# Optimization experiments

Hardware: AMD Instinct MI355X
Metric: run time of the kernel (lower is better)

## Reference

```python
import jax, jax.numpy as jnp
import numpy as np

H = 64  # hidden_size
IN = 1  # input_size
OUT = 7  # output_size
B, T = 4096, 512


def setup_inputs() -> dict:
    key = jax.random.key(0)
    ks = jax.random.split(key, 11)
    s = 1.0 / np.sqrt(H)  # PyTorch LSTM init scale
    u = lambda k, shp: jax.random.uniform(k, shp, jnp.float32, -s, s)
    return {
        "x": jax.random.normal(ks[0], (B, T, IN), jnp.float32),
        # layer 0
        "Wih0": u(ks[1], (4 * H, IN)),
        "Whh0": u(ks[2], (4 * H, H)),
        "bih0": u(ks[3], (4 * H,)),
        "bhh0": u(ks[4], (4 * H,)),
        # layer 1
        "Wih1": u(ks[5], (4 * H, H)),
        "Whh1": u(ks[6], (4 * H, H)),
        "bih1": u(ks[7], (4 * H,)),
        "bhh1": u(ks[8], (4 * H,)),
        # fc head
        "Wfc": u(ks[9], (OUT, H)),
        "bfc": u(ks[10], (OUT,)),
    }


def _lstm_layer(x, Wih, Whh, bih, bhh):
    """x: [B, T, F] -> hidden sequence [B, T, H]. PyTorch gate order i,f,g,o."""
    b, t, _ = x.shape
    h = Whh.shape[1]
    # precompute input contribution for all timesteps: [T, B, 4H]
    xg = (jnp.einsum('btf,gf->btg', x, Wih) + bih + bhh).transpose(1, 0, 2)
    WhhT = Whh.T  # [H, 4H]

    def step(carry, g_t):
        h_t, c_t = carry
        gates = g_t + h_t @ WhhT  # [B, 4H]
        i, f, g, o = jnp.split(gates, 4, axis=-1)
        i = jax.nn.sigmoid(i)
        f = jax.nn.sigmoid(f)
        g = jnp.tanh(g)
        o = jax.nn.sigmoid(o)
        c_new = f * c_t + i * g
        h_new = o * jnp.tanh(c_new)
        return (h_new, c_new), h_new

    h0 = jnp.zeros((b, h), x.dtype)
    c0 = jnp.zeros((b, h), x.dtype)
    (_, _), hs = jax.lax.scan(step, (h0, c0), xg)
    return hs.transpose(1, 0, 2)  # [B, T, H]


def reference(x, Wih0, Whh0, bih0, bhh0, Wih1, Whh1, bih1, bhh1, Wfc, bfc):
    h1 = _lstm_layer(x, Wih0, Whh0, bih0, bhh0)   # dropout between layers is identity in eval
    h2 = _lstm_layer(h1, Wih1, Whh1, bih1, bhh1)
    last = h2[:, -1, :]  # [B, H]; dropout identity in eval
    return last @ Wfc.T + bfc  # [B, OUT]
```

## Files before the change

### kernel.cpp

```cpp
#include <hip/hip_runtime.h>
#include <hip/hip_bf16.h>

#define HH 64
#define TT 512
#define BB 8

typedef __attribute__((ext_vector_type(8))) short short8;
typedef __attribute__((ext_vector_type(4))) float f32x4;

static __device__ __forceinline__ unsigned short f2bf(float f) {
  unsigned u = __float_as_uint(f);
  u += 0x7fffu + ((u >> 16) & 1u);
  return (unsigned short)(u >> 16);
}

static __device__ __forceinline__ float sigm(float x) {
  float e = __builtin_amdgcn_exp2f(-1.442695041f * x);
  return __builtin_amdgcn_rcpf(1.0f + e);
}
static __device__ __forceinline__ float tanh_fast(float x) {
  float e = __builtin_amdgcn_exp2f(2.885390082f * x);
  return 1.0f - 2.0f * __builtin_amdgcn_rcpf(1.0f + e);
}

static __device__ __forceinline__ short8 pack8(const float* __restrict__ p) {
  const float4* p4 = (const float4*)p;
  float4 a = p4[0], b = p4[1];
  short8 r;
  r[0] = (short)f2bf(a.x); r[1] = (short)f2bf(a.y);
  r[2] = (short)f2bf(a.z); r[3] = (short)f2bf(a.w);
  r[4] = (short)f2bf(b.x); r[5] = (short)f2bf(b.y);
  r[6] = (short)f2bf(b.z); r[7] = (short)f2bf(b.w);
  return r;
}

#define MF(A, B, C) __builtin_amdgcn_mfma_f32_16x16x32_bf16((A), (B), (C), 0, 0, 0)

#define ACT_STORE(A0, A1, A2, A3, J, XV, HASX, CSTv, WROv, WRB, LASTF) {       \
    float pi = (A0)[J], pf = (A1)[J], pg = (A2)[J], po = (A3)[J];              \
    if (HASX) {                                                                \
      pi = fmaf((XV), wx[0], pi); pf = fmaf((XV), wx[1], pf);                  \
      pg = fmaf((XV), wx[2], pg); po = fmaf((XV), wx[3], po);                  \
    }                                                                          \
    float iv = sigm(pi), fv = sigm(pf);                                        \
    float gv = tanh_fast(pg), ov = sigm(po);                                   \
    float c = fmaf(fv, (CSTv), iv * gv);                                       \
    (CSTv) = c;                                                                \
    float h = ov * tanh_fast(c);                                               \
    *(__hip_bfloat16*)((WRB) + (WROv)) = __float2bfloat16(h);                  \
    if (LASTF) h1f[(2 * q + (J) / 2) * HH + colw] = h;                         \
  }

#define STEP_A(P) {                                                            \
    const char* rd = (const char*)h0buf[(P) ^ 1];                              \
    short8 af0 = *(const short8*)(rd + rdo0);                                  \
    short8 af1 = *(const short8*)(rd + rdo1);                                  \
    float2 xv = *(const float2*)xpf; xpf += BB;                                \
    f32x4 a0 = MF(af0, wf[0], bs[0]); a0 = MF(af1, wf[1], a0);                 \
    f32x4 a1 = MF(af0, wf[2], bs[1]); a1 = MF(af1, wf[3], a1);                 \
    f32x4 a2 = MF(af0, wf[4], bs[2]); a2 = MF(af1, wf[5], a2);                 \
    f32x4 a3 = MF(af0, wf[6], bs[3]); a3 = MF(af1, wf[7], a3);                 \
    char* wrb = (char*)h0buf[P];                                               \
    ACT_STORE(a0, a1, a2, a3, 0, xv.x, true, cst0, wro0, wrb, false)           \
    ACT_STORE(a0, a1, a2, a3, 2, xv.y, true, cst1, wro1, wrb, false)           \
  }

#define STEP_B(P, LAST) {                                                      \
    const char* rd0 = (const char*)h0buf[(P) ^ 1];                             \
    const char* rd1 = (const char*)h1buf[P];                                   \
    short8 af0 = *(const short8*)(rd0 + rdo0);                                 \
    short8 af1 = *(const short8*)(rd0 + rdo1);                                 \
    short8 af2 = *(const short8*)(rd1 + rdo0);                                 \
    short8 af3 = *(const short8*)(rd1 + rdo1);                                 \
    f32x4 a0 = MF(af0, wf[0],  bs[0]); a0 = MF(af1, wf[1],  a0);               \
    a0 = MF(af2, wf[2],  a0);  a0 = MF(af3, wf[3],  a0);                       \
    f32x4 a1 = MF(af0, wf[4],  bs[1]); a1 = MF(af1, wf[5],  a1);               \
    a1 = MF(af2, wf[6],  a1);  a1 = MF(af3, wf[7],  a1);                       \
    f32x4 a2 = MF(af0, wf[8],  bs[2]); a2 = MF(af1, wf[9],  a2);               \
    a2 = MF(af2, wf[10], a2);  a2 = MF(af3, wf[11], a2);                       \
    f32x4 a3 = MF(af0, wf[12], bs[3]); a3 = MF(af1, wf[13], a3);               \
    a3 = MF(af2, wf[14], a3);  a3 = MF(af3, wf[15], a3);                       \
    char* wrb = (char*)h1buf[(P) ^ 1];                                         \
    ACT_STORE(a0, a1, a2, a3, 0, 0.f, false, cst0, wro0, wrb, LAST)            \
    ACT_STORE(a0, a1, a2, a3, 2, 0.f, false, cst1, wro1, wrb, LAST)            \
  }

__global__ __launch_bounds__(512, 4)
void lstm2_fused(const float* __restrict__ x,
                 const float* __restrict__ Wih0, const float* __restrict__ Whh0,
                 const float* __restrict__ bih0, const float* __restrict__ bhh0,
                 const float* __restrict__ Wih1, const float* __restrict__ Whh1,
                 const float* __restrict__ bih1, const float* __restrict__ bhh1,
                 const float* __restrict__ Wfc,  const float* __restrict__ bfc,
                 float* __restrict__ out)
{
  __shared__ float xs[TT * BB];
  __shared__ __align__(16) unsigned short h0buf[2][16 * HH];
  __shared__ __align__(16) unsigned short h1buf[2][16 * HH];
  __shared__ float h1f[BB * HH];

  const int tid  = threadIdx.x;
  const int wave = tid >> 6;
  const int lane = tid & 63;
  const int grp  = wave >> 2;
  const int w    = wave & 3;
  const int m    = lane & 15;
  const int q    = lane >> 4;
  const int b0   = blockIdx.x * BB;

  {
    const int t = tid;
    #pragma unroll
    for (int r = 0; r < BB; ++r)
      xs[t * BB + r] = x[(size_t)(b0 + r) * TT + t];
  }
  ((unsigned int*)h0buf)[tid] = 0; ((unsigned int*)h0buf)[tid + 512] = 0;
  ((unsigned int*)h1buf)[tid] = 0; ((unsigned int*)h1buf)[tid + 512] = 0;

  short8 wf[16];
  f32x4 bs[4];
  float wx[4];
  #pragma unroll
  for (int n = 0; n < 4; ++n) {
    const int colg = 16 * (4 * n + w) + m;
    if (grp == 0) {
      const float b = bih0[colg] + bhh0[colg];
      bs[n][0] = b; bs[n][1] = b; bs[n][2] = b; bs[n][3] = b;
      wx[n] = Wih0[colg];
      #pragma unroll
      for (int kt = 0; kt < 2; ++kt)
        wf[n * 2 + kt] = pack8(Whh0 + colg * HH + kt * 32 + q * 8);
    } else {
      const float b = bih1[colg] + bhh1[colg];
      bs[n][0] = b; bs[n][1] = b; bs[n][2] = b; bs[n][3] = b;
      wx[n] = 0.f;
      #pragma unroll
      for (int kt = 0; kt < 4; ++kt) {
        const float* Wsrc = (kt < 2) ? Wih1 : Whh1;
        wf[n * 4 + kt] = pack8(Wsrc + colg * HH + (kt & 1) * 32 + q * 8);
      }
    }
  }

  const int colw = 16 * w + m;
  const int rdo0 = m * 128 + ((q * 16) ^ ((m & 7) << 4));
  const int rdo1 = m * 128 + ((64 + q * 16) ^ ((m & 7) << 4));
  const int r0 = 4 * q;
  const int r2 = 4 * q + 2;
  const int wro0 = r0 * 128 + ((2 * colw) ^ ((r0 & 7) << 4));
  const int wro1 = r2 * 128 + ((2 * colw) ^ ((r2 & 7) << 4));

  __syncthreads();

  float cst0 = 0.f, cst1 = 0.f;
  const float* xpf = xs + 2 * q;

  if (grp == 0) { STEP_A(0) }
  __syncthreads();

  #pragma unroll 1
  for (int k = 0; k < (TT - 2) / 2; ++k) {
    if (grp == 0) { STEP_A(1) } else { STEP_B(1, false) }
    __syncthreads();
    if (grp == 0) { STEP_A(0) } else { STEP_B(0, false) }
    __syncthreads();
  }
  if (grp == 0) { STEP_A(1) } else { STEP_B(1, false) }
  __syncthreads();
  if (grp == 1) { STEP_B(0, true) }
  __syncthreads();

  if (tid < BB * 7) {
    const int b = tid / 7, o = tid % 7;
    float s = bfc[o];
    #pragma unroll
    for (int k = 0; k < HH; ++k) s = fmaf(h1f[b * HH + k], Wfc[o * HH + k], s);
    out[(size_t)(b0 + b) * 7 + o] = s;
  }
}

extern "C" void kernel_launch(void* const* d_in, const int* in_sizes, int n_in,
                              void* d_out, int out_size, void* d_ws, size_t ws_size,
                              hipStream_t stream) {
  const float* x    = (const float*)d_in[0];
  const float* Wih0 = (const float*)d_in[1];
  const float* Whh0 = (const float*)d_in[2];
  const float* bih0 = (const float*)d_in[3];
  const float* bhh0 = (const float*)d_in[4];
  const float* Wih1 = (const float*)d_in[5];
  const float* Whh1 = (const float*)d_in[6];
  const float* bih1 = (const float*)d_in[7];
  const float* bhh1 = (const float*)d_in[8];
  const float* Wfc  = (const float*)d_in[9];
  const float* bfc  = (const float*)d_in[10];
  float* out = (float*)d_out;

  dim3 grid(4096 / BB);
  dim3 block(512);
  hipLaunchKernelGGL(lstm2_fused, grid, block, 0, stream,
                     x, Wih0, Whh0, bih0, bhh0, Wih1, Whh1, bih1, bhh1, Wfc, bfc, out);
}
```

Before: 426.3 us.

## Merge both LSTM layers into each wave and fold activation scaling into weights

Each of 4 waves now computes both layer 0 and layer 1 for its columns, replacing the two 4-wave groups, so the block shrinks from 512 to 256 threads. The log2(e) and 2*log2(e) factors are folded into the bf16 weights and biases. The gate activations are rewritten with exp2 and combined rationals that use fewer reciprocals, processed as 2-wide vectors. The goal is to cut transcendental and reciprocal count and barrier participants, at the cost of more registers per wave, a longer serial path per wave, and possible precision changes from the clamped exponentials.

```diff
diff --git a/kernel.cpp b/kernel.cpp
--- a/kernel.cpp
+++ b/kernel.cpp
@@ -7,6 +7,10 @@
 
 typedef __attribute__((ext_vector_type(8))) short short8;
 typedef __attribute__((ext_vector_type(4))) float f32x4;
+typedef __attribute__((ext_vector_type(2))) float f32x2;
+
+#define K1 1.4426950408889634f
+#define K2 2.8853900817779268f
 
 static __device__ __forceinline__ unsigned short f2bf(float f) {
   unsigned u = __float_as_uint(f);
@@ -14,78 +18,90 @@
   return (unsigned short)(u >> 16);
 }
 
-static __device__ __forceinline__ float sigm(float x) {
-  float e = __builtin_amdgcn_exp2f(-1.442695041f * x);
-  return __builtin_amdgcn_rcpf(1.0f + e);
-}
-static __device__ __forceinline__ float tanh_fast(float x) {
-  float e = __builtin_amdgcn_exp2f(2.885390082f * x);
-  return 1.0f - 2.0f * __builtin_amdgcn_rcpf(1.0f + e);
-}
-
-static __device__ __forceinline__ short8 pack8(const float* __restrict__ p) {
-  const float4* p4 = (const float4*)p;
-  float4 a = p4[0], b = p4[1];
+static __device__ __forceinline__ short8 pack8s(const float* __restrict__ p, float s) {
   short8 r;
-  r[0] = (short)f2bf(a.x); r[1] = (short)f2bf(a.y);
-  r[2] = (short)f2bf(a.z); r[3] = (short)f2bf(a.w);
-  r[4] = (short)f2bf(b.x); r[5] = (short)f2bf(b.y);
-  r[6] = (short)f2bf(b.z); r[7] = (short)f2bf(b.w);
+  #pragma unroll
+  for (int i = 0; i < 8; ++i) r[i] = (short)f2bf(p[i] * s);
   return r;
 }
 
+static __device__ __forceinline__ f32x2 splat2(float b) { f32x2 r; r[0] = b; r[1] = b; return r; }
+static __device__ __forceinline__ f32x2 vexp2(f32x2 v) {
+  f32x2 r; r[0] = __builtin_amdgcn_exp2f(v[0]); r[1] = __builtin_amdgcn_exp2f(v[1]); return r;
+}
+static __device__ __forceinline__ f32x2 vrcp(f32x2 v) {
+  f32x2 r; r[0] = __builtin_amdgcn_rcpf(v[0]); r[1] = __builtin_amdgcn_rcpf(v[1]); return r;
+}
+static __device__ __forceinline__ f32x2 vmin(f32x2 a, float b) {
+  return __builtin_elementwise_min(a, splat2(b));
+}
+
+static __device__ __forceinline__ f32x2 lstm_act2(f32x2 zi, f32x2 zf, f32x2 zg,
+                                                  f32x2 zo, f32x2& c) {
+  f32x2 Ei = vexp2(vmin(zi, 16.f));
+  f32x2 Ef = vexp2(vmin(zf, 16.f));
+  f32x2 G  = vexp2(vmin(zg, 23.f));
+  f32x2 Eo = vexp2(vmin(zo, 16.f));
+  f32x2 Pi = Ei + 1.f, Pf = Ef + 1.f, Pg = G + 1.f, Gm = G - 1.f;
+  f32x2 t2 = Pi * Pg;
+  f32x2 N  = Ef * c * t2 + Ei * Gm * Pf;
+  f32x2 D  = Pf * t2;
+  c = N * vrcp(D);
+  f32x2 C2 = vexp2(vmin(c * K2, 23.f));
+  f32x2 num = Eo * (C2 - 1.f);
+  f32x2 den = (Eo + 1.f) * (C2 + 1.f);
+  return num * vrcp(den);
+}
+
 #define MF(A, B, C) __builtin_amdgcn_mfma_f32_16x16x32_bf16((A), (B), (C), 0, 0, 0)
 
-#define ACT_STORE(A0, A1, A2, A3, J, XV, HASX, CSTv, WROv, WRB, LASTF) {       \
-    float pi = (A0)[J], pf = (A1)[J], pg = (A2)[J], po = (A3)[J];              \
-    if (HASX) {                                                                \
-      pi = fmaf((XV), wx[0], pi); pf = fmaf((XV), wx[1], pf);                  \
-      pg = fmaf((XV), wx[2], pg); po = fmaf((XV), wx[3], po);                  \
+#define STEP(P, DO_A, DO_B, LASTF) {                                           \
+    const char* h0r = (const char*)h0buf[(P) ^ 1];                             \
+    const char* h1r = (const char*)h1buf[P];                                   \
+    short8 af0 = *(const short8*)(h0r + rdo0);                                 \
+    short8 af1 = *(const short8*)(h0r + rdo1);                                 \
+    short8 af2 = *(const short8*)(h1r + rdo0);                                 \
+    short8 af3 = *(const short8*)(h1r + rdo1);                                 \
+    if (DO_A) {                                                                \
+      f32x4 a0 = MF(af0, wfA[0], bsA[0]); a0 = MF(af1, wfA[1], a0);            \
+      f32x4 a1 = MF(af0, wfA[2], bsA[1]); a1 = MF(af1, wfA[3], a1);            \
+      f32x4 a2 = MF(af0, wfA[4], bsA[2]); a2 = MF(af1, wfA[5], a2);            \
+      f32x4 a3 = MF(af0, wfA[6], bsA[3]); a3 = MF(af1, wfA[7], a3);            \
+      f32x2 xv = *(const f32x2*)xpf; xpf += BB;                                \
+      f32x2 zi = {a0[0], a0[2]}; zi += xv * wxs[0];                            \
+      f32x2 zf = {a1[0], a1[2]}; zf += xv * wxs[1];                            \
+      f32x2 zg = {a2[0], a2[2]}; zg += xv * wxs[2];                            \
+      f32x2 zo = {a3[0], a3[2]}; zo += xv * wxs[3];                            \
+      f32x2 hA = lstm_act2(zi, zf, zg, zo, cA);                                \
+      char* h0w = (char*)h0buf[P];                                             \
+      *(__hip_bfloat16*)(h0w + wro0) = __float2bfloat16(hA[0]);                \
+      *(__hip_bfloat16*)(h0w + wro1) = __float2bfloat16(hA[1]);                \
     }                                                                          \
-    float iv = sigm(pi), fv = sigm(pf);                                        \
-    float gv = tanh_fast(pg), ov = sigm(po);                                   \
-    float c = fmaf(fv, (CSTv), iv * gv);                                       \
-    (CSTv) = c;                                                                \
-    float h = ov * tanh_fast(c);                                               \
-    *(__hip_bfloat16*)((WRB) + (WROv)) = __float2bfloat16(h);                  \
-    if (LASTF) h1f[(2 * q + (J) / 2) * HH + colw] = h;                         \
-  }
-
-#define STEP_A(P) {                                                            \
-    const char* rd = (const char*)h0buf[(P) ^ 1];                              \
-    short8 af0 = *(const short8*)(rd + rdo0);                                  \
-    short8 af1 = *(const short8*)(rd + rdo1);                                  \
-    float2 xv = *(const float2*)xpf; xpf += BB;                                \
-    f32x4 a0 = MF(af0, wf[0], bs[0]); a0 = MF(af1, wf[1], a0);                 \
-    f32x4 a1 = MF(af0, wf[2], bs[1]); a1 = MF(af1, wf[3], a1);                 \
-    f32x4 a2 = MF(af0, wf[4], bs[2]); a2 = MF(af1, wf[5], a2);                 \
-    f32x4 a3 = MF(af0, wf[6], bs[3]); a3 = MF(af1, wf[7], a3);                 \
-    char* wrb = (char*)h0buf[P];                                               \
-    ACT_STORE(a0, a1, a2, a3, 0, xv.x, true, cst0, wro0, wrb, false)           \
-    ACT_STORE(a0, a1, a2, a3, 2, xv.y, true, cst1, wro1, wrb, false)           \
-  }
-
-#define STEP_B(P, LAST) {                                                      \
-    const char* rd0 = (const char*)h0buf[(P) ^ 1];                             \
-    const char* rd1 = (const char*)h1buf[P];                                   \
-    short8 af0 = *(const short8*)(rd0 + rdo0);                                 \
-    short8 af1 = *(const short8*)(rd0 + rdo1);                                 \
-    short8 af2 = *(const short8*)(rd1 + rdo0);                                 \
-    short8 af3 = *(const short8*)(rd1 + rdo1);                                 \
-    f32x4 a0 = MF(af0, wf[0],  bs[0]); a0 = MF(af1, wf[1],  a0);               \
-    a0 = MF(af2, wf[2],  a0);  a0 = MF(af3, wf[3],  a0);                       \
-    f32x4 a1 = MF(af0, wf[4],  bs[1]); a1 = MF(af1, wf[5],  a1);               \
-    a1 = MF(af2, wf[6],  a1);  a1 = MF(af3, wf[7],  a1);                       \
-    f32x4 a2 = MF(af0, wf[8],  bs[2]); a2 = MF(af1, wf[9],  a2);               \
-    a2 = MF(af2, wf[10], a2);  a2 = MF(af3, wf[11], a2);                       \
-    f32x4 a3 = MF(af0, wf[12], bs[3]); a3 = MF(af1, wf[13], a3);               \
-    a3 = MF(af2, wf[14], a3);  a3 = MF(af3, wf[15], a3);                       \
-    char* wrb = (char*)h1buf[(P) ^ 1];                                         \
-    ACT_STORE(a0, a1, a2, a3, 0, 0.f, false, cst0, wro0, wrb, LAST)            \
-    ACT_STORE(a0, a1, a2, a3, 2, 0.f, false, cst1, wro1, wrb, LAST)            \
-  }
-
-__global__ __launch_bounds__(512, 4)
+    if (DO_B) {                                                                \
+      f32x4 b0 = MF(af0, wfB[0],  bsB[0]); b0 = MF(af1, wfB[1],  b0);          \
+      b0 = MF(af2, wfB[2],  b0);  b0 = MF(af3, wfB[3],  b0);                   \
+      f32x4 b1 = MF(af0, wfB[4],  bsB[1]); b1 = MF(af1, wfB[5],  b1);          \
+      b1 = MF(af2, wfB[6],  b1);  b1 = MF(af3, wfB[7],  b1);                   \
+      f32x4 b2 = MF(af0, wfB[8],  bsB[2]); b2 = MF(af1, wfB[9],  b2);          \
+      b2 = MF(af2, wfB[10], b2);  b2 = MF(af3, wfB[11], b2);                   \
+      f32x4 b3 = MF(af0, wfB[12], bsB[3]); b3 = MF(af1, wfB[13], b3);          \
+      b3 = MF(af2, wfB[14], b3);  b3 = MF(af3, wfB[15], b3);                   \
+      f32x2 wi = {b0[0], b0[2]};                                               \
+      f32x2 wff = {b1[0], b1[2]};                                              \
+      f32x2 wg = {b2[0], b2[2]};                                               \
+      f32x2 wo = {b3[0], b3[2]};                                               \
+      f32x2 hB = lstm_act2(wi, wff, wg, wo, cB);                               \
+      char* h1w = (char*)h1buf[(P) ^ 1];                                       \
+      *(__hip_bfloat16*)(h1w + wro0) = __float2bfloat16(hB[0]);                \
+      *(__hip_bfloat16*)(h1w + wro1) = __float2bfloat16(hB[1]);                \
+      if (LASTF) {                                                             \
+        h1f[(2 * q) * HH + colw]     = hB[0];                                  \
+        h1f[(2 * q + 1) * HH + colw] = hB[1];                                  \
+      }                                                                        \
+    }                                                                          \
+  }
+
+__global__ __launch_bounds__(256, 2)
 void lstm2_fused(const float* __restrict__ x,
                  const float* __restrict__ Wih0, const float* __restrict__ Whh0,
                  const float* __restrict__ bih0, const float* __restrict__ bhh0,
@@ -102,42 +118,43 @@
   const int tid  = threadIdx.x;
   const int wave = tid >> 6;
   const int lane = tid & 63;
-  const int grp  = wave >> 2;
-  const int w    = wave & 3;
+  const int w    = wave;
   const int m    = lane & 15;
   const int q    = lane >> 4;
   const int b0   = blockIdx.x * BB;
 
-  {
-    const int t = tid;
+  for (int t = tid; t < TT; t += 256) {
     #pragma unroll
     for (int r = 0; r < BB; ++r)
       xs[t * BB + r] = x[(size_t)(b0 + r) * TT + t];
   }
-  ((unsigned int*)h0buf)[tid] = 0; ((unsigned int*)h0buf)[tid + 512] = 0;
-  ((unsigned int*)h1buf)[tid] = 0; ((unsigned int*)h1buf)[tid + 512] = 0;
-
-  short8 wf[16];
-  f32x4 bs[4];
-  float wx[4];
+  #pragma unroll
+  for (int i = 0; i < 4; ++i) ((unsigned int*)h0buf)[tid + 256 * i] = 0;
+  #pragma unroll
+  for (int i = 0; i < 4; ++i) ((unsigned int*)h1buf)[tid + 256 * i] = 0;
+
+  short8 wfA[8], wfB[16];
+  f32x4 bsA[4], bsB[4];
+  f32x2 wxs[4];
   #pragma unroll
   for (int n = 0; n < 4; ++n) {
+    const float s = (n == 2) ? K2 : K1;
     const int colg = 16 * (4 * n + w) + m;
-    if (grp == 0) {
-      const float b = bih0[colg] + bhh0[colg];
-      bs[n][0] = b; bs[n][1] = b; bs[n][2] = b; bs[n][3] = b;
-      wx[n] = Wih0[colg];
+    {
+      const float b = (bih0[colg] + bhh0[colg]) * s;
+      bsA[n][0] = b; bsA[n][1] = b; bsA[n][2] = b; bsA[n][3] = b;
+      wxs[n] = splat2(Wih0[colg] * s);
       #pragma unroll
       for (int kt = 0; kt < 2; ++kt)
-        wf[n * 2 + kt] = pack8(Whh0 + colg * HH + kt * 32 + q * 8);
-    } else {
-      const float b = bih1[colg] + bhh1[colg];
-      bs[n][0] = b; bs[n][1] = b; bs[n][2] = b; bs[n][3] = b;
-      wx[n] = 0.f;
+        wfA[n * 2 + kt] = pack8s(Whh0 + colg * HH + kt * 32 + q * 8, s);
+    }
+    {
+      const float b = (bih1[colg] + bhh1[colg]) * s;
+      bsB[n][0] = b; bsB[n][1] = b; bsB[n][2] = b; bsB[n][3] = b;
       #pragma unroll
       for (int kt = 0; kt < 4; ++kt) {
         const float* Wsrc = (kt < 2) ? Wih1 : Whh1;
-        wf[n * 4 + kt] = pack8(Wsrc + colg * HH + (kt & 1) * 32 + q * 8);
+        wfB[n * 4 + kt] = pack8s(Wsrc + colg * HH + (kt & 1) * 32 + q * 8, s);
       }
     }
   }
@@ -152,22 +169,22 @@
 
   __syncthreads();
 
-  float cst0 = 0.f, cst1 = 0.f;
+  f32x2 cA = splat2(0.f), cB = splat2(0.f);
   const float* xpf = xs + 2 * q;
 
-  if (grp == 0) { STEP_A(0) }
+  STEP(0, true, false, false)
   __syncthreads();
 
   #pragma unroll 1
   for (int k = 0; k < (TT - 2) / 2; ++k) {
-    if (grp == 0) { STEP_A(1) } else { STEP_B(1, false) }
+    STEP(1, true, true, false)
     __syncthreads();
-    if (grp == 0) { STEP_A(0) } else { STEP_B(0, false) }
+    STEP(0, true, true, false)
     __syncthreads();
   }
-  if (grp == 0) { STEP_A(1) } else { STEP_B(1, false) }
-  __syncthreads();
-  if (grp == 1) { STEP_B(0, true) }
+  STEP(1, true, true, false)
+  __syncthreads();
+  STEP(0, false, true, true)
   __syncthreads();
 
   if (tid < BB * 7) {
@@ -196,7 +213,7 @@
   float* out = (float*)d_out;
 
   dim3 grid(4096 / BB);
-  dim3 block(512);
+  dim3 block(256);
   hipLaunchKernelGGL(lstm2_fused, grid, block, 0, stream,
                      x, Wih0, Whh0, bih0, bhh0, Wih1, Whh1, bih1, bhh1, Wfc, bfc, out);
 }
```

After: 466.0 us. 1.09x slower.

## Fill all 16 MFMA rows with batch and fuse LSTM activations algebraically

Applied to the files above, without the earlier changes.

Doubles the batch tile per block from 8 to 16, so all 16 M-rows of the 16x16x32 MFMA carry real batch rows instead of half being wasted. The grid halves and each lane now updates four cell states. The gate activations are rewritten as a single rational expression built from exp2 results, which cuts the number of reciprocals per cell. The log2(e) scale factors are folded into the weights and biases at load time, and the math runs on packed float2 vectors. The trade-offs are fewer blocks per CU to hide the serial recurrence latency, and clamps on the exponent inputs to avoid overflow.

```diff
diff --git a/kernel.cpp b/kernel.cpp
--- a/kernel.cpp
+++ b/kernel.cpp
@@ -3,10 +3,14 @@
 
 #define HH 64
 #define TT 512
-#define BB 8
+#define BB 16
 
 typedef __attribute__((ext_vector_type(8))) short short8;
 typedef __attribute__((ext_vector_type(4))) float f32x4;
+typedef __attribute__((ext_vector_type(2))) float f32x2;
+
+#define K1 1.4426950408889634f
+#define K2 2.8853900817779268f
 
 static __device__ __forceinline__ unsigned short f2bf(float f) {
   unsigned u = __float_as_uint(f);
@@ -14,55 +18,73 @@
   return (unsigned short)(u >> 16);
 }
 
-static __device__ __forceinline__ float sigm(float x) {
-  float e = __builtin_amdgcn_exp2f(-1.442695041f * x);
-  return __builtin_amdgcn_rcpf(1.0f + e);
-}
-static __device__ __forceinline__ float tanh_fast(float x) {
-  float e = __builtin_amdgcn_exp2f(2.885390082f * x);
-  return 1.0f - 2.0f * __builtin_amdgcn_rcpf(1.0f + e);
-}
-
-static __device__ __forceinline__ short8 pack8(const float* __restrict__ p) {
-  const float4* p4 = (const float4*)p;
-  float4 a = p4[0], b = p4[1];
+static __device__ __forceinline__ short8 pack8s(const float* __restrict__ p, float s) {
   short8 r;
-  r[0] = (short)f2bf(a.x); r[1] = (short)f2bf(a.y);
-  r[2] = (short)f2bf(a.z); r[3] = (short)f2bf(a.w);
-  r[4] = (short)f2bf(b.x); r[5] = (short)f2bf(b.y);
-  r[6] = (short)f2bf(b.z); r[7] = (short)f2bf(b.w);
+  #pragma unroll
+  for (int i = 0; i < 8; ++i) r[i] = (short)f2bf(p[i] * s);
   return r;
 }
 
+static __device__ __forceinline__ f32x2 splat2(float b) { f32x2 r; r[0] = b; r[1] = b; return r; }
+static __device__ __forceinline__ f32x2 vexp2(f32x2 v) {
+  f32x2 r; r[0] = __builtin_amdgcn_exp2f(v[0]); r[1] = __builtin_amdgcn_exp2f(v[1]); return r;
+}
+static __device__ __forceinline__ f32x2 vrcp(f32x2 v) {
+  f32x2 r; r[0] = __builtin_amdgcn_rcpf(v[0]); r[1] = __builtin_amdgcn_rcpf(v[1]); return r;
+}
+static __device__ __forceinline__ f32x2 vmin2(f32x2 a, float b) {
+  return __builtin_elementwise_min(a, splat2(b));
+}
+
+static __device__ __forceinline__ f32x2 lstm_act2(f32x2 zi, f32x2 zf, f32x2 zg,
+                                                  f32x2 zo, f32x2& c) {
+  f32x2 Ei = vexp2(vmin2(zi, 16.f));
+  f32x2 Ef = vexp2(vmin2(zf, 16.f));
+  f32x2 G  = vexp2(vmin2(zg, 23.f));
+  f32x2 Eo = vexp2(vmin2(zo, 16.f));
+  f32x2 Pi = Ei + 1.f, Pf = Ef + 1.f, Pg = G + 1.f, Gm = G - 1.f;
+  f32x2 t2 = Pi * Pg;
+  f32x2 N  = Ef * c * t2 + Ei * Gm * Pf;
+  f32x2 D  = Pf * t2;
+  c = N * vrcp(D);
+  f32x2 C2 = vexp2(vmin2(c * K2, 23.f));
+  f32x2 num = Eo * (C2 - 1.f);
+  f32x2 den = (Eo + 1.f) * (C2 + 1.f);
+  return num * vrcp(den);
+}
+
 #define MF(A, B, C) __builtin_amdgcn_mfma_f32_16x16x32_bf16((A), (B), (C), 0, 0, 0)
-
-#define ACT_STORE(A0, A1, A2, A3, J, XV, HASX, CSTv, WROv, WRB, LASTF) {       \
-    float pi = (A0)[J], pf = (A1)[J], pg = (A2)[J], po = (A3)[J];              \
-    if (HASX) {                                                                \
-      pi = fmaf((XV), wx[0], pi); pf = fmaf((XV), wx[1], pf);                  \
-      pg = fmaf((XV), wx[2], pg); po = fmaf((XV), wx[3], po);                  \
-    }                                                                          \
-    float iv = sigm(pi), fv = sigm(pf);                                        \
-    float gv = tanh_fast(pg), ov = sigm(po);                                   \
-    float c = fmaf(fv, (CSTv), iv * gv);                                       \
-    (CSTv) = c;                                                                \
-    float h = ov * tanh_fast(c);                                               \
-    *(__hip_bfloat16*)((WRB) + (WROv)) = __float2bfloat16(h);                  \
-    if (LASTF) h1f[(2 * q + (J) / 2) * HH + colw] = h;                         \
-  }
 
 #define STEP_A(P) {                                                            \
     const char* rd = (const char*)h0buf[(P) ^ 1];                              \
     short8 af0 = *(const short8*)(rd + rdo0);                                  \
     short8 af1 = *(const short8*)(rd + rdo1);                                  \
-    float2 xv = *(const float2*)xpf; xpf += BB;                                \
+    f32x4 xv = *(const f32x4*)xpf; xpf += BB;                                  \
     f32x4 a0 = MF(af0, wf[0], bs[0]); a0 = MF(af1, wf[1], a0);                 \
     f32x4 a1 = MF(af0, wf[2], bs[1]); a1 = MF(af1, wf[3], a1);                 \
     f32x4 a2 = MF(af0, wf[4], bs[2]); a2 = MF(af1, wf[5], a2);                 \
     f32x4 a3 = MF(af0, wf[6], bs[3]); a3 = MF(af1, wf[7], a3);                 \
     char* wrb = (char*)h0buf[P];                                               \
-    ACT_STORE(a0, a1, a2, a3, 0, xv.x, true, cst0, wro0, wrb, false)           \
-    ACT_STORE(a0, a1, a2, a3, 2, xv.y, true, cst1, wro1, wrb, false)           \
+    {                                                                          \
+      f32x2 xp2 = {xv[0], xv[1]};                                              \
+      f32x2 zi = {a0[0], a0[1]}; zi += xp2 * wxs[0];                           \
+      f32x2 zf = {a1[0], a1[1]}; zf += xp2 * wxs[1];                           \
+      f32x2 zg = {a2[0], a2[1]}; zg += xp2 * wxs[2];                           \
+      f32x2 zo = {a3[0], a3[1]}; zo += xp2 * wxs[3];                           \
+      f32x2 h2 = lstm_act2(zi, zf, zg, zo, cst01);                             \
+      *(__hip_bfloat16*)(wrb + wro[0]) = __float2bfloat16(h2[0]);              \
+      *(__hip_bfloat16*)(wrb + wro[1]) = __float2bfloat16(h2[1]);              \
+    }                                                                          \
+    {                                                                          \
+      f32x2 xp2 = {xv[2], xv[3]};                                              \
+      f32x2 zi = {a0[2], a0[3]}; zi += xp2 * wxs[0];                           \
+      f32x2 zf = {a1[2], a1[3]}; zf += xp2 * wxs[1];                           \
+      f32x2 zg = {a2[2], a2[3]}; zg += xp2 * wxs[2];                           \
+      f32x2 zo = {a3[2], a3[3]}; zo += xp2 * wxs[3];                           \
+      f32x2 h2 = lstm_act2(zi, zf, zg, zo, cst23);                             \
+      *(__hip_bfloat16*)(wrb + wro[2]) = __float2bfloat16(h2[0]);              \
+      *(__hip_bfloat16*)(wrb + wro[3]) = __float2bfloat16(h2[1]);              \
+    }                                                                          \
   }
 
 #define STEP_B(P, LAST) {                                                      \
@@ -81,11 +103,31 @@
     f32x4 a3 = MF(af0, wf[12], bs[3]); a3 = MF(af1, wf[13], a3);               \
     a3 = MF(af2, wf[14], a3);  a3 = MF(af3, wf[15], a3);                       \
     char* wrb = (char*)h1buf[(P) ^ 1];                                         \
-    ACT_STORE(a0, a1, a2, a3, 0, 0.f, false, cst0, wro0, wrb, LAST)            \
-    ACT_STORE(a0, a1, a2, a3, 2, 0.f, false, cst1, wro1, wrb, LAST)            \
-  }
-
-__global__ __launch_bounds__(512, 4)
+    {                                                                          \
+      f32x2 zi = {a0[0], a0[1]}, zf = {a1[0], a1[1]};                          \
+      f32x2 zg = {a2[0], a2[1]}, zo = {a3[0], a3[1]};                          \
+      f32x2 h2 = lstm_act2(zi, zf, zg, zo, cst01);                             \
+      *(__hip_bfloat16*)(wrb + wro[0]) = __float2bfloat16(h2[0]);              \
+      *(__hip_bfloat16*)(wrb + wro[1]) = __float2bfloat16(h2[1]);              \
+      if (LAST) {                                                              \
+        h1f[(q * 4 + 0) * HH + colw] = h2[0];                                  \
+        h1f[(q * 4 + 1) * HH + colw] = h2[1];                                  \
+      }                                                                        \
+    }                                                                          \
+    {                                                                          \
+      f32x2 zi = {a0[2], a0[3]}, zf = {a1[2], a1[3]};                          \
+      f32x2 zg = {a2[2], a2[3]}, zo = {a3[2], a3[3]};                          \
+      f32x2 h2 = lstm_act2(zi, zf, zg, zo, cst23);                             \
+      *(__hip_bfloat16*)(wrb + wro[2]) = __float2bfloat16(h2[0]);              \
+      *(__hip_bfloat16*)(wrb + wro[3]) = __float2bfloat16(h2[1]);              \
+      if (LAST) {                                                              \
+        h1f[(q * 4 + 2) * HH + colw] = h2[0];                                  \
+        h1f[(q * 4 + 3) * HH + colw] = h2[1];                                  \
+      }                                                                        \
+    }                                                                          \
+  }
+
+__global__ __launch_bounds__(512, 2)
 void lstm2_fused(const float* __restrict__ x,
                  const float* __restrict__ Wih0, const float* __restrict__ Whh0,
                  const float* __restrict__ bih0, const float* __restrict__ bhh0,
@@ -95,8 +137,8 @@
                  float* __restrict__ out)
 {
   __shared__ float xs[TT * BB];
-  __shared__ __align__(16) unsigned short h0buf[2][16 * HH];
-  __shared__ __align__(16) unsigned short h1buf[2][16 * HH];
+  __shared__ __align__(16) unsigned short h0buf[2][BB * HH];
+  __shared__ __align__(16) unsigned short h1buf[2][BB * HH];
   __shared__ float h1f[BB * HH];
 
   const int tid  = threadIdx.x;
@@ -119,25 +161,26 @@
 
   short8 wf[16];
   f32x4 bs[4];
-  float wx[4];
+  f32x2 wxs[4];
   #pragma unroll
   for (int n = 0; n < 4; ++n) {
+    const float s = (n == 2) ? K2 : K1;
     const int colg = 16 * (4 * n + w) + m;
     if (grp == 0) {
-      const float b = bih0[colg] + bhh0[colg];
+      const float b = (bih0[colg] + bhh0[colg]) * s;
       bs[n][0] = b; bs[n][1] = b; bs[n][2] = b; bs[n][3] = b;
-      wx[n] = Wih0[colg];
+      wxs[n] = splat2(Wih0[colg] * s);
       #pragma unroll
       for (int kt = 0; kt < 2; ++kt)
-        wf[n * 2 + kt] = pack8(Whh0 + colg * HH + kt * 32 + q * 8);
+        wf[n * 2 + kt] = pack8s(Whh0 + colg * HH + kt * 32 + q * 8, s);
     } else {
-      const float b = bih1[colg] + bhh1[colg];
+      const float b = (bih1[colg] + bhh1[colg]) * s;
       bs[n][0] = b; bs[n][1] = b; bs[n][2] = b; bs[n][3] = b;
-      wx[n] = 0.f;
+      wxs[n] = splat2(0.f);
       #pragma unroll
       for (int kt = 0; kt < 4; ++kt) {
         const float* Wsrc = (kt < 2) ? Wih1 : Whh1;
-        wf[n * 4 + kt] = pack8(Wsrc + colg * HH + (kt & 1) * 32 + q * 8);
+        wf[n * 4 + kt] = pack8s(Wsrc + colg * HH + (kt & 1) * 32 + q * 8, s);
       }
     }
   }
@@ -145,15 +188,17 @@
   const int colw = 16 * w + m;
   const int rdo0 = m * 128 + ((q * 16) ^ ((m & 7) << 4));
   const int rdo1 = m * 128 + ((64 + q * 16) ^ ((m & 7) << 4));
-  const int r0 = 4 * q;
-  const int r2 = 4 * q + 2;
-  const int wro0 = r0 * 128 + ((2 * colw) ^ ((r0 & 7) << 4));
-  const int wro1 = r2 * 128 + ((2 * colw) ^ ((r2 & 7) << 4));
-
-  __syncthreads();
-
-  float cst0 = 0.f, cst1 = 0.f;
-  const float* xpf = xs + 2 * q;
+  int wro[4];
+  #pragma unroll
+  for (int j = 0; j < 4; ++j) {
+    const int row = q * 4 + j;
+    wro[j] = row * 128 + ((2 * colw) ^ ((row & 7) << 4));
+  }
+
+  __syncthreads();
+
+  f32x2 cst01 = splat2(0.f), cst23 = splat2(0.f);
+  const float* xpf = xs + q * 4;
 
   if (grp == 0) { STEP_A(0) }
   __syncthreads();
```

Result: faster. 369.0 us, median of 3 (-13.4%).

## Fill MFMA rows with 16 batch rows and fuse LSTM activation math

Applied to the files above, without the earlier changes.

Doubles the batch rows per block from 8 to 16, so the previously padded half of each 16x16 MFMA tile now does useful work, and halves the grid. The x·Wih0 input term moves into an extra MFMA using a bf16 one-hot A fragment, and weights and biases are pre-scaled by log2e constants so gate exponentials need no multiply. The activations become one vectorised routine that merges the sigmoid and tanh reciprocals into fewer rcp calls, with clamps to avoid overflow. s_setprio is raised around the MFMA chains. In exchange, occupancy bounds drop to 2 blocks per CU, leaving fewer waves to hide the serial step latency, and the merged reciprocal formula adds rounding differences.

```diff
diff --git a/kernel.cpp b/kernel.cpp
--- a/kernel.cpp
+++ b/kernel.cpp
@@ -3,10 +3,14 @@
 
 #define HH 64
 #define TT 512
-#define BB 8
+#define BB 16
 
 typedef __attribute__((ext_vector_type(8))) short short8;
 typedef __attribute__((ext_vector_type(4))) float f32x4;
+typedef __attribute__((ext_vector_type(4))) int int4v;
+
+#define K1 1.4426950408889634f
+#define K2 2.8853900817779268f
 
 static __device__ __forceinline__ unsigned short f2bf(float f) {
   unsigned u = __float_as_uint(f);
@@ -14,55 +18,76 @@
   return (unsigned short)(u >> 16);
 }
 
-static __device__ __forceinline__ float sigm(float x) {
-  float e = __builtin_amdgcn_exp2f(-1.442695041f * x);
-  return __builtin_amdgcn_rcpf(1.0f + e);
-}
-static __device__ __forceinline__ float tanh_fast(float x) {
-  float e = __builtin_amdgcn_exp2f(2.885390082f * x);
-  return 1.0f - 2.0f * __builtin_amdgcn_rcpf(1.0f + e);
-}
-
-static __device__ __forceinline__ short8 pack8(const float* __restrict__ p) {
-  const float4* p4 = (const float4*)p;
-  float4 a = p4[0], b = p4[1];
+static __device__ __forceinline__ short8 pack8s(const float* __restrict__ p, float s) {
   short8 r;
-  r[0] = (short)f2bf(a.x); r[1] = (short)f2bf(a.y);
-  r[2] = (short)f2bf(a.z); r[3] = (short)f2bf(a.w);
-  r[4] = (short)f2bf(b.x); r[5] = (short)f2bf(b.y);
-  r[6] = (short)f2bf(b.z); r[7] = (short)f2bf(b.w);
+  #pragma unroll
+  for (int i = 0; i < 8; ++i) r[i] = (short)f2bf(p[i] * s);
   return r;
 }
 
+static __device__ __forceinline__ f32x4 splat4(float b) {
+  f32x4 r; r[0] = b; r[1] = b; r[2] = b; r[3] = b; return r;
+}
+static __device__ __forceinline__ f32x4 vexp4(f32x4 v) {
+  f32x4 r;
+  r[0] = __builtin_amdgcn_exp2f(v[0]); r[1] = __builtin_amdgcn_exp2f(v[1]);
+  r[2] = __builtin_amdgcn_exp2f(v[2]); r[3] = __builtin_amdgcn_exp2f(v[3]);
+  return r;
+}
+static __device__ __forceinline__ f32x4 vrcp4(f32x4 v) {
+  f32x4 r;
+  r[0] = __builtin_amdgcn_rcpf(v[0]); r[1] = __builtin_amdgcn_rcpf(v[1]);
+  r[2] = __builtin_amdgcn_rcpf(v[2]); r[3] = __builtin_amdgcn_rcpf(v[3]);
+  return r;
+}
+static __device__ __forceinline__ f32x4 vmin4(f32x4 a, float b) {
+  return __builtin_elementwise_min(a, splat4(b));
+}
+
+static __device__ __forceinline__ f32x4 lstm_act4(f32x4 zi, f32x4 zf, f32x4 zg,
+                                                  f32x4 zo, f32x4& c) {
+  f32x4 Ei = vexp4(vmin4(zi, 16.f));
+  f32x4 Ef = vexp4(vmin4(zf, 16.f));
+  f32x4 G  = vexp4(vmin4(zg, 23.f));
+  f32x4 Eo = vexp4(vmin4(zo, 16.f));
+  f32x4 Pi = Ei + 1.f, Pf = Ef + 1.f, Pg = G + 1.f, Gm = G - 1.f;
+  f32x4 t2 = Pi * Pg;
+  f32x4 N  = Ef * c * t2 + Ei * Gm * Pf;
+  f32x4 D  = Pf * t2;
+  c = N * vrcp4(D);
+  f32x4 C2 = vexp4(vmin4(c * K2, 23.f));
+  f32x4 num = Eo * (C2 - 1.f);
+  f32x4 den = (Eo + 1.f) * (C2 + 1.f);
+  return num * vrcp4(den);
+}
+
 #define MF(A, B, C) __builtin_amdgcn_mfma_f32_16x16x32_bf16((A), (B), (C), 0, 0, 0)
-
-#define ACT_STORE(A0, A1, A2, A3, J, XV, HASX, CSTv, WROv, WRB, LASTF) {       \
-    float pi = (A0)[J], pf = (A1)[J], pg = (A2)[J], po = (A3)[J];              \
-    if (HASX) {                                                                \
-      pi = fmaf((XV), wx[0], pi); pf = fmaf((XV), wx[1], pf);                  \
-      pg = fmaf((XV), wx[2], pg); po = fmaf((XV), wx[3], po);                  \
-    }                                                                          \
-    float iv = sigm(pi), fv = sigm(pf);                                        \
-    float gv = tanh_fast(pg), ov = sigm(po);                                   \
-    float c = fmaf(fv, (CSTv), iv * gv);                                       \
-    (CSTv) = c;                                                                \
-    float h = ov * tanh_fast(c);                                               \
-    *(__hip_bfloat16*)((WRB) + (WROv)) = __float2bfloat16(h);                  \
-    if (LASTF) h1f[(2 * q + (J) / 2) * HH + colw] = h;                         \
-  }
 
 #define STEP_A(P) {                                                            \
     const char* rd = (const char*)h0buf[(P) ^ 1];                              \
     short8 af0 = *(const short8*)(rd + rdo0);                                  \
     short8 af1 = *(const short8*)(rd + rdo1);                                  \
-    float2 xv = *(const float2*)xpf; xpf += BB;                                \
-    f32x4 a0 = MF(af0, wf[0], bs[0]); a0 = MF(af1, wf[1], a0);                 \
-    f32x4 a1 = MF(af0, wf[2], bs[1]); a1 = MF(af1, wf[3], a1);                 \
-    f32x4 a2 = MF(af0, wf[4], bs[2]); a2 = MF(af1, wf[5], a2);                 \
-    f32x4 a3 = MF(af0, wf[6], bs[3]); a3 = MF(af1, wf[7], a3);                 \
+    float xval = *xpf; xpf += BB;                \
+    __hip_bfloat16 xb = __float2bfloat16(xval);                                \
+    unsigned short xu; __builtin_memcpy(&xu, &xb, 2);                          \
+    int4v xi = {q0 ? (int)xu : 0, 0, 0, 0};                                    \
+    short8 afx; __builtin_memcpy(&afx, &xi, 16);                               \
+    __builtin_amdgcn_s_setprio(1);                                             \
+    f32x4 a0 = MF(afx, wfx[0], bs[0]);                                         \
+    f32x4 a1 = MF(afx, wfx[1], bs[1]);                                         \
+    f32x4 a2 = MF(afx, wfx[2], bs[2]);                                         \
+    f32x4 a3 = MF(afx, wfx[3], bs[3]);                                         \
+    a0 = MF(af0, wf[0], a0); a0 = MF(af1, wf[1], a0);                          \
+    a1 = MF(af0, wf[2], a1); a1 = MF(af1, wf[3], a1);                          \
+    a2 = MF(af0, wf[4], a2); a2 = MF(af1, wf[5], a2);                          \
+    a3 = MF(af0, wf[6], a3); a3 = MF(af1, wf[7], a3);                          \
+    __builtin_amdgcn_s_setprio(0);                                             \
+    f32x4 h4 = lstm_act4(a0, a1, a2, a3, cstv);                                \
     char* wrb = (char*)h0buf[P];                                               \
-    ACT_STORE(a0, a1, a2, a3, 0, xv.x, true, cst0, wro0, wrb, false)           \
-    ACT_STORE(a0, a1, a2, a3, 2, xv.y, true, cst1, wro1, wrb, false)           \
+    *(__hip_bfloat16*)(wrb + wro[0]) = __float2bfloat16(h4[0]);                \
+    *(__hip_bfloat16*)(wrb + wro[1]) = __float2bfloat16(h4[1]);                \
+    *(__hip_bfloat16*)(wrb + wro[2]) = __float2bfloat16(h4[2]);                \
+    *(__hip_bfloat16*)(wrb + wro[3]) = __float2bfloat16(h4[3]);                \
   }
 
 #define STEP_B(P, LAST) {                                                      \
@@ -72,6 +97,7 @@
     short8 af1 = *(const short8*)(rd0 + rdo1);                                 \
     short8 af2 = *(const short8*)(rd1 + rdo0);                                 \
     short8 af3 = *(const short8*)(rd1 + rdo1);                                 \
+    __builtin_amdgcn_s_setprio(1);                                             \
     f32x4 a0 = MF(af0, wf[0],  bs[0]); a0 = MF(af1, wf[1],  a0);               \
     a0 = MF(af2, wf[2],  a0);  a0 = MF(af3, wf[3],  a0);                       \
     f32x4 a1 = MF(af0, wf[4],  bs[1]); a1 = MF(af1, wf[5],  a1);               \
@@ -80,12 +106,22 @@
     a2 = MF(af2, wf[10], a2);  a2 = MF(af3, wf[11], a2);                       \
     f32x4 a3 = MF(af0, wf[12], bs[3]); a3 = MF(af1, wf[13], a3);               \
     a3 = MF(af2, wf[14], a3);  a3 = MF(af3, wf[15], a3);                       \
+    __builtin_amdgcn_s_setprio(0);                                             \
+    f32x4 h4 = lstm_act4(a0, a1, a2, a3, cstv);                                \
     char* wrb = (char*)h1buf[(P) ^ 1];                                         \
-    ACT_STORE(a0, a1, a2, a3, 0, 0.f, false, cst0, wro0, wrb, LAST)            \
-    ACT_STORE(a0, a1, a2, a3, 2, 0.f, false, cst1, wro1, wrb, LAST)            \
-  }
-
-__global__ __launch_bounds__(512, 4)
+    *(__hip_bfloat16*)(wrb + wro[0]) = __float2bfloat16(h4[0]);                \
+    *(__hip_bfloat16*)(wrb + wro[1]) = __float2bfloat16(h4[1]);                \
+    *(__hip_bfloat16*)(wrb + wro[2]) = __float2bfloat16(h4[2]);                \
+    *(__hip_bfloat16*)(wrb + wro[3]) = __float2bfloat16(h4[3]);                \
+    if (LAST) {                                                                \
+      h1f[(q * 4 + 0) * HH + colw] = h4[0];                                    \
+      h1f[(q * 4 + 1) * HH + colw] = h4[1];                                    \
+      h1f[(q * 4 + 2) * HH + colw] = h4[2];                                    \
+      h1f[(q * 4 + 3) * HH + colw] = h4[3];                                    \
+    }                                                                          \
+  }
+
+__global__ __launch_bounds__(512, 2)
 void lstm2_fused(const float* __restrict__ x,
                  const float* __restrict__ Wih0, const float* __restrict__ Whh0,
                  const float* __restrict__ bih0, const float* __restrict__ bhh0,
@@ -95,8 +131,8 @@
                  float* __restrict__ out)
 {
   __shared__ float xs[TT * BB];
-  __shared__ __align__(16) unsigned short h0buf[2][16 * HH];
-  __shared__ __align__(16) unsigned short h1buf[2][16 * HH];
+  __shared__ __align__(16) unsigned short h0buf[2][BB * HH];
+  __shared__ __align__(16) unsigned short h1buf[2][BB * HH];
   __shared__ float h1f[BB * HH];
 
   const int tid  = threadIdx.x;
@@ -106,6 +142,7 @@
   const int w    = wave & 3;
   const int m    = lane & 15;
   const int q    = lane >> 4;
+  const bool q0  = (q == 0);
   const int b0   = blockIdx.x * BB;
 
   {
@@ -117,27 +154,27 @@
   ((unsigned int*)h0buf)[tid] = 0; ((unsigned int*)h0buf)[tid + 512] = 0;
   ((unsigned int*)h1buf)[tid] = 0; ((unsigned int*)h1buf)[tid + 512] = 0;
 
-  short8 wf[16];
+  short8 wf[16], wfx[4];
   f32x4 bs[4];
-  float wx[4];
   #pragma unroll
   for (int n = 0; n < 4; ++n) {
+    const float s = (n == 2) ? K2 : K1;
     const int colg = 16 * (4 * n + w) + m;
     if (grp == 0) {
-      const float b = bih0[colg] + bhh0[colg];
-      bs[n][0] = b; bs[n][1] = b; bs[n][2] = b; bs[n][3] = b;
-      wx[n] = Wih0[colg];
+      bs[n] = splat4((bih0[colg] + bhh0[colg]) * s);
+      int4v wi = {q0 ? (int)f2bf(Wih0[colg] * s) : 0, 0, 0, 0};
+      __builtin_memcpy(&wfx[n], &wi, 16);
       #pragma unroll
       for (int kt = 0; kt < 2; ++kt)
-        wf[n * 2 + kt] = pack8(Whh0 + colg * HH + kt * 32 + q * 8);
+        wf[n * 2 + kt] = pack8s(Whh0 + colg * HH + kt * 32 + q * 8, s);
     } else {
-      const float b = bih1[colg] + bhh1[colg];
-      bs[n][0] = b; bs[n][1] = b; bs[n][2] = b; bs[n][3] = b;
-      wx[n] = 0.f;
+      bs[n] = splat4((bih1[colg] + bhh1[colg]) * s);
+      int4v wi = {0, 0, 0, 0};
+      __builtin_memcpy(&wfx[n], &wi, 16);
       #pragma unroll
       for (int kt = 0; kt < 4; ++kt) {
         const float* Wsrc = (kt < 2) ? Wih1 : Whh1;
-        wf[n * 4 + kt] = pack8(Wsrc + colg * HH + (kt & 1) * 32 + q * 8);
+        wf[n * 4 + kt] = pack8s(Wsrc + colg * HH + (kt & 1) * 32 + q * 8, s);
       }
     }
   }
@@ -145,15 +182,17 @@
   const int colw = 16 * w + m;
   const int rdo0 = m * 128 + ((q * 16) ^ ((m & 7) << 4));
   const int rdo1 = m * 128 + ((64 + q * 16) ^ ((m & 7) << 4));
-  const int r0 = 4 * q;
-  const int r2 = 4 * q + 2;
-  const int wro0 = r0 * 128 + ((2 * colw) ^ ((r0 & 7) << 4));
-  const int wro1 = r2 * 128 + ((2 * colw) ^ ((r2 & 7) << 4));
-
-  __syncthreads();
-
-  float cst0 = 0.f, cst1 = 0.f;
-  const float* xpf = xs + 2 * q;
+  int wro[4];
+  #pragma unroll
+  for (int j = 0; j < 4; ++j) {
+    const int row = q * 4 + j;
+    wro[j] = row * 128 + ((2 * colw) ^ ((row & 7) << 4));
+  }
+
+  __syncthreads();
+
+  f32x4 cstv = splat4(0.f);
+  const float* xpf = xs + m;
 
   if (grp == 0) { STEP_A(0) }
   __syncthreads();
```

Measured after the change: 378.5 us. 1.13x faster.
